# Kernel optimization log

Measured on AMD Instinct MI355X. Metric: run time of the kernel, lower is better.

Reference implementation:

```python
import jax, jax.numpy as jnp
import numpy as np

N_TOKENS = 8192
D_MODEL = 1024
D_HIDDEN = 4096
N_EXPERTS = 8
TOP_K = 2


def setup_inputs() -> dict:
    key = jax.random.key(0)
    ks = jax.random.split(key, 7)
    s = 0.02
    return {
        "x": jax.random.normal(ks[0], (N_TOKENS, D_MODEL), dtype=jnp.float32),
        "gate_w": jax.random.normal(ks[1], (D_MODEL, N_EXPERTS), dtype=jnp.float32) * s,
        "gate_b": jnp.zeros((N_EXPERTS,), dtype=jnp.float32),
        "w1": jax.random.normal(ks[2], (N_EXPERTS, D_MODEL, D_HIDDEN), dtype=jnp.float32) * s,
        "b1": jnp.zeros((N_EXPERTS, D_HIDDEN), dtype=jnp.float32),
        "w2": jax.random.normal(ks[3], (N_EXPERTS, D_HIDDEN, D_MODEL), dtype=jnp.float32) * s,
        "b2": jnp.zeros((N_EXPERTS, D_MODEL), dtype=jnp.float32),
    }


def reference(x, gate_w, gate_b, w1, b1, w2, b2):
    # Gating: softmax over experts, then top-k routing
    gate_scores = jax.nn.softmax(x @ gate_w + gate_b, axis=-1)        # [N, E]
    topk_vals, topk_idx = jax.lax.top_k(gate_scores, TOP_K)          # [N, K]

    # Combine weights: sum of topk_vals scattered to expert slots
    onehot = jax.nn.one_hot(topk_idx, N_EXPERTS, dtype=x.dtype)      # [N, K, E]
    combine = jnp.einsum('nk,nke->ne', topk_vals, onehot)            # [N, E]

    # Dense expert evaluation (math identical to masked dispatch: unselected
    # experts receive weight 0 in `combine`).
    h = jax.nn.relu(jnp.einsum('nd,edh->neh', x, w1) + b1)           # [N, E, H]
    expert_out = jnp.einsum('neh,ehd->ned', h, w2) + b2              # [N, E, D]
    output = jnp.einsum('ned,ne->nd', expert_out, combine)           # [N, D]

    # Load-balancing loss from routing counts
    load = jnp.sum(onehot, axis=(0, 1))                              # [E]
    load_balancing_loss = jnp.sum((load / jnp.sum(load)) ** 2)
    return output, load_balancing_loss
```

## Files before the change

kernel.cpp:

```cpp
#include <hip/hip_runtime.h>

#define D_MODEL   1024
#define D_HIDDEN  4096
#define N_EXPERTS 8
#define N_TOKENS  8192
#define NASSIGN   (N_TOKENS * 2)
#define PADCAP    (NASSIGN + N_EXPERTS * 256)
#define RT_TILES  (PADCAP / 256)

typedef unsigned short u16;
typedef __bf16 bf16x8 __attribute__((ext_vector_type(8)));
typedef float  f32x4  __attribute__((ext_vector_type(4)));

__device__ __forceinline__ u16 f2bf(float f) {
  union { float f; unsigned u; } c; c.f = f;
  unsigned u = c.u;
  u = (u + 0x7fffu + ((u >> 16) & 1u)) >> 16;
  return (u16)u;
}

__device__ __forceinline__ void async16(const void* g, void* l) {
  __builtin_amdgcn_global_load_lds(
      (const __attribute__((address_space(1))) unsigned int*)g,
      (__attribute__((address_space(3))) unsigned int*)l, 16, 0, 0);
}

#define MFMA(a, b, c) __builtin_amdgcn_mfma_f32_16x16x32_bf16((a), (b), (c), 0, 0, 0)

#define WAIT8_BARRIER() asm volatile("s_waitcnt vmcnt(8)\n\ts_barrier" ::: "memory")
#define WAIT0_BARRIER() asm volatile("s_waitcnt vmcnt(0)\n\ts_barrier" ::: "memory")
#define BARRIER()       asm volatile("s_barrier" ::: "memory")

__global__ __launch_bounds__(256) void gating_kernel(
    const float* __restrict__ x, const float* __restrict__ gw,
    const float* __restrict__ gb, int* __restrict__ counts,
    int* __restrict__ tok_idx, float* __restrict__ tok_w)
{
  const int n = blockIdx.x * 4 + (threadIdx.x >> 6);
  const int lane = threadIdx.x & 63;
  float acc[8] = {0.f,0.f,0.f,0.f,0.f,0.f,0.f,0.f};
  for (int d = lane; d < D_MODEL; d += 64) {
    float xv = x[(size_t)n * D_MODEL + d];
    const float4* g = (const float4*)&gw[d * 8];
    float4 g0 = g[0], g1 = g[1];
    acc[0] += xv * g0.x; acc[1] += xv * g0.y; acc[2] += xv * g0.z; acc[3] += xv * g0.w;
    acc[4] += xv * g1.x; acc[5] += xv * g1.y; acc[6] += xv * g1.z; acc[7] += xv * g1.w;
  }
  for (int off = 32; off; off >>= 1)
    #pragma unroll
    for (int e = 0; e < 8; ++e) acc[e] += __shfl_xor(acc[e], off, 64);
  if (lane == 0) {
    float l[8], p[8];
    float m = -1e30f;
    for (int e = 0; e < 8; ++e) { l[e] = acc[e] + gb[e]; m = fmaxf(m, l[e]); }
    float s = 0.f;
    for (int e = 0; e < 8; ++e) { p[e] = expf(l[e] - m); s += p[e]; }
    float inv = 1.f / s;
    for (int e = 0; e < 8; ++e) p[e] *= inv;
    int i0 = 0;
    for (int e = 1; e < 8; ++e) if (p[e] > p[i0]) i0 = e;
    int i1 = (i0 == 0) ? 1 : 0;
    for (int e = 0; e < 8; ++e) if (e != i0 && p[e] > p[i1]) i1 = e;
    tok_idx[2 * n]     = i0;  tok_idx[2 * n + 1] = i1;
    tok_w[2 * n]       = p[i0]; tok_w[2 * n + 1] = p[i1];
    atomicAdd(&counts[i0], 1);
    atomicAdd(&counts[i1], 1);
  }
}

__global__ void finalize_routing(const int* __restrict__ counts,
                                 int* __restrict__ offsets,
                                 float* __restrict__ out_loss)
{
  int off = 0;
  for (int e = 0; e < 8; ++e) {
    offsets[e] = off;
    off += ((counts[e] + 255) >> 8) << 8;
  }
  offsets[8] = off;
  float loss = 0.f;
  for (int e = 0; e < 8; ++e) {
    float f = (float)counts[e] * (1.f / (float)NASSIGN);
    loss += f * f;
  }
  *out_loss = loss;
}

__global__ __launch_bounds__(256) void scatter_kernel(
    const int* __restrict__ tok_idx, const float* __restrict__ tok_w,
    const int* __restrict__ offsets, int* __restrict__ cursors,
    int* __restrict__ assign_token, float* __restrict__ assign_w,
    int* __restrict__ tok_pos)
{
  const int n = blockIdx.x * 256 + threadIdx.x;
  #pragma unroll
  for (int k = 0; k < 2; ++k) {
    int e = tok_idx[n * 2 + k];
    int pos = offsets[e] + atomicAdd(&cursors[e], 1);
    assign_token[pos] = n;
    assign_w[pos] = tok_w[n * 2 + k];
    tok_pos[n * 2 + k] = pos;
  }
}

__global__ __launch_bounds__(256) void convert_x_kernel(
    const float* __restrict__ x, u16* __restrict__ xb)
{
  size_t i = ((size_t)blockIdx.x * 256 + threadIdx.x) * 4;
  float4 v = *(const float4*)&x[i];
  unsigned lo = (unsigned)f2bf(v.x) | ((unsigned)f2bf(v.y) << 16);
  unsigned hi = (unsigned)f2bf(v.z) | ((unsigned)f2bf(v.w) << 16);
  uint2 o; o.x = lo; o.y = hi;
  *(uint2*)&xb[i] = o;
}

__global__ __launch_bounds__(256) void transpose_cvt_kernel(
    const float* __restrict__ in, u16* __restrict__ out, int R, int C)
{
  const int e = blockIdx.z;
  const int c0 = blockIdx.x * 32, r0 = blockIdx.y * 32;
  __shared__ float tile[32][33];
  const int tx = threadIdx.x & 31, ty = threadIdx.x >> 5;
  const float* ip = in + (size_t)e * R * C;
  u16* op = out + (size_t)e * R * C;
  #pragma unroll
  for (int i = 0; i < 4; ++i)
    tile[ty + i * 8][tx] = ip[(size_t)(r0 + ty + i * 8) * C + c0 + tx];
  __syncthreads();
  #pragma unroll
  for (int i = 0; i < 4; ++i)
    op[(size_t)(c0 + ty + i * 8) * R + r0 + tx] = f2bf(tile[tx][ty + i * 8]);
}


__global__ __launch_bounds__(512, 2) void gemm1_kernel(
    const u16* __restrict__ xb, const u16* __restrict__ w1t,
    const float* __restrict__ b1, const int* __restrict__ assign_token,
    const int* __restrict__ offsets, u16* __restrict__ hbuf)
{
  const int rtl = (blockIdx.x & 7) * 9 + (blockIdx.x >> 3);
  const int ct = blockIdx.y;
  if (rtl * 256 >= offsets[8]) return;
  int e = 0;
  while (offsets[e + 1] <= rtl * 256) ++e;

  __shared__ __align__(16) u16 smem[65536];

  const int tid = threadIdx.x;
  const int wave = tid >> 6, lane = tid & 63;
  const int wm = wave >> 2, wn = wave & 3;

  const int r0 = tid >> 2, s0 = (tid & 3) ^ ((r0 >> 1) & 3);
  const int r1 = r0 + 128, s1 = (tid & 3) ^ ((r1 >> 1) & 3);
  const long aS0 = (long)assign_token[rtl * 256 + r0] * D_MODEL + s0 * 8;
  const long aS1 = (long)assign_token[rtl * 256 + r1] * D_MODEL + s1 * 8;
  const long bS0 = ((long)e * D_HIDDEN + ct * 256 + r0) * D_MODEL + s0 * 8;
  const long bS1 = ((long)e * D_HIDDEN + ct * 256 + r1) * D_MODEL + s1 * 8;

  f32x4 acc[8][4];
  #pragma unroll
  for (int i = 0; i < 8; ++i)
    #pragma unroll
    for (int j = 0; j < 4; ++j) acc[i][j] = (f32x4){0.f, 0.f, 0.f, 0.f};

  int aoff[8], boff[4];
  #pragma unroll
  for (int f = 0; f < 8; ++f) {
    int row = wm * 128 + f * 16 + (lane & 15);
    aoff[f] = row * 32 + (((lane >> 4) ^ ((row >> 1) & 3)) * 8);
  }
  #pragma unroll
  for (int f = 0; f < 4; ++f) {
    int col = wn * 64 + f * 16 + (lane & 15);
    boff[f] = 32768 + col * 32 + (((lane >> 4) ^ ((col >> 1) & 3)) * 8);
  }

  #define STG1(d, h, koff) do { \
    u16* A_ = &smem[((d) * 2 + (h)) * 8192 + wave * 512]; \
    u16* B_ = &smem[32768 + ((d) * 2 + (h)) * 8192 + wave * 512]; \
    async16(xb  + aS0 + (koff), A_); \
    async16(xb  + aS1 + (koff), A_ + 4096); \
    async16(w1t + bS0 + (koff), B_); \
    async16(w1t + bS1 + (koff), B_ + 4096); \
  } while (0)

  const int NT = D_MODEL / 64;
  STG1(0, 0, 0);
  STG1(0, 1, 32);
  STG1(1, 0, 64);

  for (int t = 0; t < NT; ++t) {
    const int d = t & 1;
    const int reg0 = d * 16384, reg1 = d * 16384 + 8192;
    bf16x8 a[8], b0, b1r;
    if (t + 1 < NT) WAIT8_BARRIER();
    else            WAIT0_BARRIER();
    #pragma unroll
    for (int f = 0; f < 8; ++f) a[f] = *(const bf16x8*)&smem[reg0 + aoff[f]];
    b0 = *(const bf16x8*)&smem[reg0 + boff[0]];
    b1r = *(const bf16x8*)&smem[reg0 + boff[1]];
    if (t + 1 < NT) STG1(d ^ 1, 1, (t + 1) * 64 + 32);
    __builtin_amdgcn_s_setprio(1);
    #pragma unroll
    for (int f = 0; f < 8; ++f) {
      acc[f][0] = MFMA(a[f], b0, acc[f][0]);
      acc[f][1] = MFMA(a[f], b1r, acc[f][1]);
    }
    __builtin_amdgcn_s_setprio(0);
    BARRIER();
    b0 = *(const bf16x8*)&smem[reg0 + boff[2]];
    b1r = *(const bf16x8*)&smem[reg0 + boff[3]];
    __builtin_amdgcn_s_setprio(1);
    #pragma unroll
    for (int f = 0; f < 8; ++f) {
      acc[f][2] = MFMA(a[f], b0, acc[f][2]);
      acc[f][3] = MFMA(a[f], b1r, acc[f][3]);
    }
    __builtin_amdgcn_s_setprio(0);
    if (t + 1 < NT) WAIT8_BARRIER();
    else            WAIT0_BARRIER();
    #pragma unroll
    for (int f = 0; f < 8; ++f) a[f] = *(const bf16x8*)&smem[reg1 + aoff[f]];
    b0 = *(const bf16x8*)&smem[reg1 + boff[0]];
    b1r = *(const bf16x8*)&smem[reg1 + boff[1]];
    if (t + 2 < NT) STG1(d, 0, (t + 2) * 64);
    __builtin_amdgcn_s_setprio(1);
    #pragma unroll
    for (int f = 0; f < 8; ++f) {
      acc[f][0] = MFMA(a[f], b0, acc[f][0]);
      acc[f][1] = MFMA(a[f], b1r, acc[f][1]);
    }
    __builtin_amdgcn_s_setprio(0);
    BARRIER();
    b0 = *(const bf16x8*)&smem[reg1 + boff[2]];
    b1r = *(const bf16x8*)&smem[reg1 + boff[3]];
    __builtin_amdgcn_s_setprio(1);
    #pragma unroll
    for (int f = 0; f < 8; ++f) {
      acc[f][2] = MFMA(a[f], b0, acc[f][2]);
      acc[f][3] = MFMA(a[f], b1r, acc[f][3]);
    }
    __builtin_amdgcn_s_setprio(0);
  }
  #undef STG1

  float bias[4];
  #pragma unroll
  for (int j = 0; j < 4; ++j)
    bias[j] = b1[(size_t)e * D_HIDDEN + ct * 256 + wn * 64 + j * 16 + (lane & 15)];

  __syncthreads();
  u16* Hs = smem;
  #pragma unroll
  for (int i = 0; i < 8; ++i)
    #pragma unroll
    for (int j = 0; j < 4; ++j)
      #pragma unroll
      for (int r = 0; r < 4; ++r) {
        int rl = wm * 128 + i * 16 + ((lane >> 4) * 4) + r;
        int cl = wn * 64 + j * 16 + (lane & 15);
        Hs[rl * 256 + cl] = f2bf(fmaxf(acc[i][j][r] + bias[j], 0.f));
      }
  __syncthreads();
  #pragma unroll
  for (int it = 0; it < 16; ++it) {
    int cc = tid + it * 512;
    int row = cc >> 5, cs = cc & 31;
    *(uint4*)&hbuf[((size_t)(rtl * 256 + row)) * D_HIDDEN + ct * 256 + cs * 8] =
        *(const uint4*)&Hs[row * 256 + cs * 8];
  }
}

template <bool EO>
__global__ __launch_bounds__(512, 2) void gemm2_kernel(
    const u16* __restrict__ hbuf, const u16* __restrict__ w2t,
    const float* __restrict__ b2, const int* __restrict__ assign_token,
    const float* __restrict__ assign_w, const int* __restrict__ offsets,
    float* __restrict__ dst)
{
  const int rtl = (blockIdx.x & 7) * 9 + (blockIdx.x >> 3);
  const int ct = blockIdx.y;
  const int sk = blockIdx.z;
  const long skb = (long)sk * 1024;
  if (rtl * 256 >= offsets[8]) return;
  int e = 0;
  while (offsets[e + 1] <= rtl * 256) ++e;

  __shared__ __align__(16) u16 smem[65536];

  const int tid = threadIdx.x;
  const int wave = tid >> 6, lane = tid & 63;
  const int wm = wave >> 2, wn = wave & 3;

  const int r0 = tid >> 2, s0 = (tid & 3) ^ ((r0 >> 1) & 3);
  const int r1 = r0 + 128, s1 = (tid & 3) ^ ((r1 >> 1) & 3);
  const long aS0 = ((long)(rtl * 256 + r0)) * D_HIDDEN + s0 * 8;
  const long aS1 = ((long)(rtl * 256 + r1)) * D_HIDDEN + s1 * 8;
  const long bS0 = ((long)e * D_MODEL + ct * 256 + r0) * D_HIDDEN + s0 * 8;
  const long bS1 = ((long)e * D_MODEL + ct * 256 + r1) * D_HIDDEN + s1 * 8;

  f32x4 acc[8][4];
  #pragma unroll
  for (int i = 0; i < 8; ++i)
    #pragma unroll
    for (int j = 0; j < 4; ++j) acc[i][j] = (f32x4){0.f, 0.f, 0.f, 0.f};

  int aoff[8], boff[4];
  #pragma unroll
  for (int f = 0; f < 8; ++f) {
    int row = wm * 128 + f * 16 + (lane & 15);
    aoff[f] = row * 32 + (((lane >> 4) ^ ((row >> 1) & 3)) * 8);
  }
  #pragma unroll
  for (int f = 0; f < 4; ++f) {
    int col = wn * 64 + f * 16 + (lane & 15);
    boff[f] = 32768 + col * 32 + (((lane >> 4) ^ ((col >> 1) & 3)) * 8);
  }

  #define STG2(d, h, koff) do { \
    u16* A_ = &smem[((d) * 2 + (h)) * 8192 + wave * 512]; \
    u16* B_ = &smem[32768 + ((d) * 2 + (h)) * 8192 + wave * 512]; \
    async16(hbuf + aS0 + (koff), A_); \
    async16(hbuf + aS1 + (koff), A_ + 4096); \
    async16(w2t + bS0 + (koff), B_); \
    async16(w2t + bS1 + (koff), B_ + 4096); \
  } while (0)

  const int NT = 1024 / 64;
  STG2(0, 0, skb);
  STG2(0, 1, skb + 32);
  STG2(1, 0, skb + 64);

  for (int t = 0; t < NT; ++t) {
    const int d = t & 1;
    const int reg0 = d * 16384, reg1 = d * 16384 + 8192;
    bf16x8 a[8], b0, b1r;
    if (t + 1 < NT) WAIT8_BARRIER();
    else            WAIT0_BARRIER();
    #pragma unroll
    for (int f = 0; f < 8; ++f) a[f] = *(const bf16x8*)&smem[reg0 + aoff[f]];
    b0 = *(const bf16x8*)&smem[reg0 + boff[0]];
    b1r = *(const bf16x8*)&smem[reg0 + boff[1]];
    if (t + 1 < NT) STG2(d ^ 1, 1, skb + (t + 1) * 64 + 32);
    __builtin_amdgcn_s_setprio(1);
    #pragma unroll
    for (int f = 0; f < 8; ++f) {
      acc[f][0] = MFMA(a[f], b0, acc[f][0]);
      acc[f][1] = MFMA(a[f], b1r, acc[f][1]);
    }
    __builtin_amdgcn_s_setprio(0);
    BARRIER();
    b0 = *(const bf16x8*)&smem[reg0 + boff[2]];
    b1r = *(const bf16x8*)&smem[reg0 + boff[3]];
    __builtin_amdgcn_s_setprio(1);
    #pragma unroll
    for (int f = 0; f < 8; ++f) {
      acc[f][2] = MFMA(a[f], b0, acc[f][2]);
      acc[f][3] = MFMA(a[f], b1r, acc[f][3]);
    }
    __builtin_amdgcn_s_setprio(0);
    if (t + 1 < NT) WAIT8_BARRIER();
    else            WAIT0_BARRIER();
    #pragma unroll
    for (int f = 0; f < 8; ++f) a[f] = *(const bf16x8*)&smem[reg1 + aoff[f]];
    b0 = *(const bf16x8*)&smem[reg1 + boff[0]];
    b1r = *(const bf16x8*)&smem[reg1 + boff[1]];
    if (t + 2 < NT) STG2(d, 0, skb + (t + 2) * 64);
    __builtin_amdgcn_s_setprio(1);
    #pragma unroll
    for (int f = 0; f < 8; ++f) {
      acc[f][0] = MFMA(a[f], b0, acc[f][0]);
      acc[f][1] = MFMA(a[f], b1r, acc[f][1]);
    }
    __builtin_amdgcn_s_setprio(0);
    BARRIER();
    b0 = *(const bf16x8*)&smem[reg1 + boff[2]];
    b1r = *(const bf16x8*)&smem[reg1 + boff[3]];
    __builtin_amdgcn_s_setprio(1);
    #pragma unroll
    for (int f = 0; f < 8; ++f) {
      acc[f][2] = MFMA(a[f], b0, acc[f][2]);
      acc[f][3] = MFMA(a[f], b1r, acc[f][3]);
    }
    __builtin_amdgcn_s_setprio(0);
  }
  #undef STG2

  float bias[4];
  #pragma unroll
  for (int j = 0; j < 4; ++j)
    bias[j] = (sk == 0) ? b2[(size_t)e * D_MODEL + ct * 256 + wn * 64 + j * 16 + (lane & 15)] : 0.f;

  __syncthreads();
  float* wsm = (float*)smem;
  int* tsm = (int*)&smem[1024];
  if (tid < 256) {
    wsm[tid] = assign_w[rtl * 256 + tid];
    tsm[tid] = assign_token[rtl * 256 + tid];
  }
  __syncthreads();

  #pragma unroll
  for (int i = 0; i < 8; ++i)
    #pragma unroll
    for (int r = 0; r < 4; ++r) {
      int rl = wm * 128 + i * 16 + ((lane >> 4) * 4) + r;
      float wgt = wsm[rl];
      if (EO) {
        size_t row = (size_t)(rtl * 256 + rl);
        #pragma unroll
        for (int j = 0; j < 4; ++j) {
          float v = (acc[i][j][r] + bias[j]) * wgt;
          atomicAdd(&dst[row * D_MODEL + ct * 256 + wn * 64 + j * 16 + (lane & 15)], v);
        }
      } else {
        int tok = tsm[rl];
        #pragma unroll
        for (int j = 0; j < 4; ++j) {
          float v = (acc[i][j][r] + bias[j]) * wgt;
          atomicAdd(&dst[(size_t)tok * D_MODEL + ct * 256 + wn * 64 + j * 16 + (lane & 15)], v);
        }
      }
    }
}

__global__ __launch_bounds__(256) void combine_kernel(
    const float* __restrict__ eo, const int* __restrict__ tok_pos,
    float* __restrict__ out)
{
  int idx = blockIdx.x * 256 + threadIdx.x;
  int n = idx >> 8;
  int c = (idx & 255) * 4;
  int p0 = tok_pos[2 * n], p1 = tok_pos[2 * n + 1];
  float4 a = *(const float4*)&eo[(size_t)p0 * D_MODEL + c];
  float4 b = *(const float4*)&eo[(size_t)p1 * D_MODEL + c];
  float4 o; o.x = a.x + b.x; o.y = a.y + b.y; o.z = a.z + b.z; o.w = a.w + b.w;
  *(float4*)&out[(size_t)n * D_MODEL + c] = o;
}

__global__ __launch_bounds__(256) void moe_fallback_kernel(
    const float* __restrict__ x, const float* __restrict__ w1,
    const float* __restrict__ b1, const float* __restrict__ w2,
    const float* __restrict__ b2, const int* __restrict__ tok_idx,
    const float* __restrict__ tok_w, float* __restrict__ out)
{
  const int a = blockIdx.x;
  const int n = a >> 1, slot = a & 1;
  const int e = tok_idx[n * 2 + slot];
  const float wgt = tok_w[n * 2 + slot];
  __shared__ float xs[D_MODEL];
  __shared__ float hs[D_HIDDEN];
  const int tid = threadIdx.x;
  for (int d = tid; d < D_MODEL; d += 256) xs[d] = x[(size_t)n * D_MODEL + d];
  __syncthreads();
  for (int h = tid; h < D_HIDDEN; h += 256) {
    float acc = b1[(size_t)e * D_HIDDEN + h];
    for (int d = 0; d < D_MODEL; ++d)
      acc += xs[d] * w1[((size_t)e * D_MODEL + d) * D_HIDDEN + h];
    hs[h] = fmaxf(acc, 0.f);
  }
  __syncthreads();
  for (int d = tid; d < D_MODEL; d += 256) {
    float acc = b2[(size_t)e * D_MODEL + d];
    for (int h = 0; h < D_HIDDEN; ++h)
      acc += hs[h] * w2[((size_t)e * D_HIDDEN + h) * D_MODEL + d];
    atomicAdd(&out[(size_t)n * D_MODEL + d], wgt * acc);
  }
}

extern "C" void kernel_launch(void* const* d_in, const int* in_sizes, int n_in,
                              void* d_out, int out_size, void* d_ws, size_t ws_size,
                              hipStream_t stream) {
  const float* x      = (const float*)d_in[0];
  const float* gate_w = (const float*)d_in[1];
  const float* gate_b = (const float*)d_in[2];
  const float* w1     = (const float*)d_in[3];
  const float* b1     = (const float*)d_in[4];
  const float* w2     = (const float*)d_in[5];
  const float* b2     = (const float*)d_in[6];
  float* out = (float*)d_out;

  char* ws = (char*)d_ws;
  int*   counts       = (int*)(ws + 0);
  int*   cursors      = (int*)(ws + 32);
  int*   offsets      = (int*)(ws + 64);
  int*   tok_idx      = (int*)(ws + 256);
  float* tok_w        = (float*)(ws + 65792);
  int*   tok_pos      = (int*)(ws + 131328);
  int*   assign_token = (int*)(ws + 196864);
  float* assign_w     = (float*)(ws + 270592);
  const size_t X0 = 344320;
  u16*   hbuf = (u16*)(ws + X0);
  u16*   xb   = (u16*)(ws + X0 + 150994944ull);
  u16*   w1t  = (u16*)(ws + X0 + 150994944ull + 16777216ull);
  u16*   w2t  = (u16*)(ws + X0 + 150994944ull);
  float* eo   = (float*)(ws + X0 + 150994944ull + 67108864ull);
  const size_t REQ_FAST = X0 + 150994944ull + 16777216ull + 67108864ull;
  const size_t REQ_EO   = X0 + 150994944ull + 67108864ull + 75497472ull;

  const bool fast = (ws_size >= REQ_FAST);
  const bool eoPath = fast && (ws_size >= REQ_EO);

  hipMemsetAsync(ws, 0, X0, stream);
  if (!eoPath) {
    hipMemsetAsync(d_out, 0, (size_t)out_size * sizeof(float), stream);
  }

  gating_kernel<<<N_TOKENS / 4, 256, 0, stream>>>(x, gate_w, gate_b, counts, tok_idx, tok_w);
  finalize_routing<<<1, 1, 0, stream>>>(counts, offsets, out + (out_size - 1));

  if (fast) {
    scatter_kernel<<<N_TOKENS / 256, 256, 0, stream>>>(tok_idx, tok_w, offsets, cursors,
                                                       assign_token, assign_w, tok_pos);
    convert_x_kernel<<<(N_TOKENS * D_MODEL) / 1024, 256, 0, stream>>>(x, xb);
    transpose_cvt_kernel<<<dim3(D_HIDDEN / 32, D_MODEL / 32, N_EXPERTS), 256, 0, stream>>>(
        w1, w1t, D_MODEL, D_HIDDEN);
    gemm1_kernel<<<dim3(RT_TILES, D_HIDDEN / 256), 512, 0, stream>>>(
        xb, w1t, b1, assign_token, offsets, hbuf);
    transpose_cvt_kernel<<<dim3(D_MODEL / 32, D_HIDDEN / 32, N_EXPERTS), 256, 0, stream>>>(
        w2, w2t, D_HIDDEN, D_MODEL);
    if (eoPath) {
      hipMemsetAsync(eo, 0, 75497472ull, stream);
      gemm2_kernel<true><<<dim3(RT_TILES, D_MODEL / 256, 4), 512, 0, stream>>>(
          hbuf, w2t, b2, assign_token, assign_w, offsets, eo);
      combine_kernel<<<(N_TOKENS * D_MODEL) / 1024, 256, 0, stream>>>(eo, tok_pos, out);
    } else {
      gemm2_kernel<false><<<dim3(RT_TILES, D_MODEL / 256, 4), 512, 0, stream>>>(
          hbuf, w2t, b2, assign_token, assign_w, offsets, out);
    }
  } else {
    moe_fallback_kernel<<<NASSIGN, 256, 0, stream>>>(x, w1, b1, w2, b2, tok_idx, tok_w, out);
  }
}
```

Baseline: 886.7 us.

## Rework GEMM pipeline barriers and halve gemm2 split-K factor

Restructures the main loop of both GEMM kernels: the wait threshold drops from vmcnt(8) to vmcnt(4), each half-stage uses separate B fragment registers (b2/b3), and extra barriers separate LDS reads from the MFMA phases and the next async stage. Gemm2's split-K factor goes from 4 to 2, so each block covers 2048 of the K dimension. The aim is tighter load/compute interleaving and fewer partial-sum atomics or stores in gemm2. The cost is more barriers per iteration and fewer gemm2 blocks, which could reduce occupancy or latency hiding.

```diff
diff --git a/kernel.cpp b/kernel.cpp
--- a/kernel.cpp
+++ b/kernel.cpp
@@ -27,7 +27,7 @@
 
 #define MFMA(a, b, c) __builtin_amdgcn_mfma_f32_16x16x32_bf16((a), (b), (c), 0, 0, 0)
 
-#define WAIT8_BARRIER() asm volatile("s_waitcnt vmcnt(8)\n\ts_barrier" ::: "memory")
+#define WAIT4_BARRIER() asm volatile("s_waitcnt vmcnt(4)\n\ts_barrier" ::: "memory")
 #define WAIT0_BARRIER() asm volatile("s_waitcnt vmcnt(0)\n\ts_barrier" ::: "memory")
 #define BARRIER()       asm volatile("s_barrier" ::: "memory")
 
@@ -188,18 +188,18 @@
   STG1(0, 0, 0);
   STG1(0, 1, 32);
   STG1(1, 0, 64);
+  WAIT4_BARRIER();
 
   for (int t = 0; t < NT; ++t) {
     const int d = t & 1;
     const int reg0 = d * 16384, reg1 = d * 16384 + 8192;
-    bf16x8 a[8], b0, b1r;
-    if (t + 1 < NT) WAIT8_BARRIER();
-    else            WAIT0_BARRIER();
+    bf16x8 a[8], b0, b1r, b2, b3;
     #pragma unroll
     for (int f = 0; f < 8; ++f) a[f] = *(const bf16x8*)&smem[reg0 + aoff[f]];
-    b0 = *(const bf16x8*)&smem[reg0 + boff[0]];
+    b0  = *(const bf16x8*)&smem[reg0 + boff[0]];
     b1r = *(const bf16x8*)&smem[reg0 + boff[1]];
     if (t + 1 < NT) STG1(d ^ 1, 1, (t + 1) * 64 + 32);
+    BARRIER();
     __builtin_amdgcn_s_setprio(1);
     #pragma unroll
     for (int f = 0; f < 8; ++f) {
@@ -208,22 +208,23 @@
     }
     __builtin_amdgcn_s_setprio(0);
     BARRIER();
-    b0 = *(const bf16x8*)&smem[reg0 + boff[2]];
-    b1r = *(const bf16x8*)&smem[reg0 + boff[3]];
-    __builtin_amdgcn_s_setprio(1);
-    #pragma unroll
-    for (int f = 0; f < 8; ++f) {
-      acc[f][2] = MFMA(a[f], b0, acc[f][2]);
-      acc[f][3] = MFMA(a[f], b1r, acc[f][3]);
-    }
-    __builtin_amdgcn_s_setprio(0);
-    if (t + 1 < NT) WAIT8_BARRIER();
-    else            WAIT0_BARRIER();
+    b2 = *(const bf16x8*)&smem[reg0 + boff[2]];
+    b3 = *(const bf16x8*)&smem[reg0 + boff[3]];
+    BARRIER();
+    __builtin_amdgcn_s_setprio(1);
+    #pragma unroll
+    for (int f = 0; f < 8; ++f) {
+      acc[f][2] = MFMA(a[f], b2, acc[f][2]);
+      acc[f][3] = MFMA(a[f], b3, acc[f][3]);
+    }
+    __builtin_amdgcn_s_setprio(0);
+    BARRIER();
     #pragma unroll
     for (int f = 0; f < 8; ++f) a[f] = *(const bf16x8*)&smem[reg1 + aoff[f]];
-    b0 = *(const bf16x8*)&smem[reg1 + boff[0]];
+    b0  = *(const bf16x8*)&smem[reg1 + boff[0]];
     b1r = *(const bf16x8*)&smem[reg1 + boff[1]];
     if (t + 2 < NT) STG1(d, 0, (t + 2) * 64);
+    BARRIER();
     __builtin_amdgcn_s_setprio(1);
     #pragma unroll
     for (int f = 0; f < 8; ++f) {
@@ -232,15 +233,18 @@
     }
     __builtin_amdgcn_s_setprio(0);
     BARRIER();
-    b0 = *(const bf16x8*)&smem[reg1 + boff[2]];
-    b1r = *(const bf16x8*)&smem[reg1 + boff[3]];
-    __builtin_amdgcn_s_setprio(1);
-    #pragma unroll
-    for (int f = 0; f < 8; ++f) {
-      acc[f][2] = MFMA(a[f], b0, acc[f][2]);
-      acc[f][3] = MFMA(a[f], b1r, acc[f][3]);
-    }
-    __builtin_amdgcn_s_setprio(0);
+    b2 = *(const bf16x8*)&smem[reg1 + boff[2]];
+    b3 = *(const bf16x8*)&smem[reg1 + boff[3]];
+    if (t < NT - 2) WAIT4_BARRIER();
+    else            WAIT0_BARRIER();
+    __builtin_amdgcn_s_setprio(1);
+    #pragma unroll
+    for (int f = 0; f < 8; ++f) {
+      acc[f][2] = MFMA(a[f], b2, acc[f][2]);
+      acc[f][3] = MFMA(a[f], b3, acc[f][3]);
+    }
+    __builtin_amdgcn_s_setprio(0);
+    BARRIER();
   }
   #undef STG1
 
@@ -281,7 +285,7 @@
   const int rtl = (blockIdx.x & 7) * 9 + (blockIdx.x >> 3);
   const int ct = blockIdx.y;
   const int sk = blockIdx.z;
-  const long skb = (long)sk * 1024;
+  const long skb = (long)sk * 2048;
   if (rtl * 256 >= offsets[8]) return;
   int e = 0;
   while (offsets[e + 1] <= rtl * 256) ++e;
@@ -326,22 +330,22 @@
     async16(w2t + bS1 + (koff), B_ + 4096); \
   } while (0)
 
-  const int NT = 1024 / 64;
+  const int NT = 2048 / 64;
   STG2(0, 0, skb);
   STG2(0, 1, skb + 32);
   STG2(1, 0, skb + 64);
+  WAIT4_BARRIER();
 
   for (int t = 0; t < NT; ++t) {
     const int d = t & 1;
     const int reg0 = d * 16384, reg1 = d * 16384 + 8192;
-    bf16x8 a[8], b0, b1r;
-    if (t + 1 < NT) WAIT8_BARRIER();
-    else            WAIT0_BARRIER();
+    bf16x8 a[8], b0, b1r, b2, b3;
     #pragma unroll
     for (int f = 0; f < 8; ++f) a[f] = *(const bf16x8*)&smem[reg0 + aoff[f]];
-    b0 = *(const bf16x8*)&smem[reg0 + boff[0]];
+    b0  = *(const bf16x8*)&smem[reg0 + boff[0]];
     b1r = *(const bf16x8*)&smem[reg0 + boff[1]];
     if (t + 1 < NT) STG2(d ^ 1, 1, skb + (t + 1) * 64 + 32);
+    BARRIER();
     __builtin_amdgcn_s_setprio(1);
     #pragma unroll
     for (int f = 0; f < 8; ++f) {
@@ -350,22 +354,23 @@
     }
     __builtin_amdgcn_s_setprio(0);
     BARRIER();
-    b0 = *(const bf16x8*)&smem[reg0 + boff[2]];
-    b1r = *(const bf16x8*)&smem[reg0 + boff[3]];
-    __builtin_amdgcn_s_setprio(1);
-    #pragma unroll
-    for (int f = 0; f < 8; ++f) {
-      acc[f][2] = MFMA(a[f], b0, acc[f][2]);
-      acc[f][3] = MFMA(a[f], b1r, acc[f][3]);
-    }
-    __builtin_amdgcn_s_setprio(0);
-    if (t + 1 < NT) WAIT8_BARRIER();
-    else            WAIT0_BARRIER();
+    b2 = *(const bf16x8*)&smem[reg0 + boff[2]];
+    b3 = *(const bf16x8*)&smem[reg0 + boff[3]];
+    BARRIER();
+    __builtin_amdgcn_s_setprio(1);
+    #pragma unroll
+    for (int f = 0; f < 8; ++f) {
+      acc[f][2] = MFMA(a[f], b2, acc[f][2]);
+      acc[f][3] = MFMA(a[f], b3, acc[f][3]);
+    }
+    __builtin_amdgcn_s_setprio(0);
+    BARRIER();
     #pragma unroll
     for (int f = 0; f < 8; ++f) a[f] = *(const bf16x8*)&smem[reg1 + aoff[f]];
-    b0 = *(const bf16x8*)&smem[reg1 + boff[0]];
+    b0  = *(const bf16x8*)&smem[reg1 + boff[0]];
     b1r = *(const bf16x8*)&smem[reg1 + boff[1]];
     if (t + 2 < NT) STG2(d, 0, skb + (t + 2) * 64);
+    BARRIER();
     __builtin_amdgcn_s_setprio(1);
     #pragma unroll
     for (int f = 0; f < 8; ++f) {
@@ -374,15 +379,18 @@
     }
     __builtin_amdgcn_s_setprio(0);
     BARRIER();
-    b0 = *(const bf16x8*)&smem[reg1 + boff[2]];
-    b1r = *(const bf16x8*)&smem[reg1 + boff[3]];
-    __builtin_amdgcn_s_setprio(1);
-    #pragma unroll
-    for (int f = 0; f < 8; ++f) {
-      acc[f][2] = MFMA(a[f], b0, acc[f][2]);
-      acc[f][3] = MFMA(a[f], b1r, acc[f][3]);
-    }
-    __builtin_amdgcn_s_setprio(0);
+    b2 = *(const bf16x8*)&smem[reg1 + boff[2]];
+    b3 = *(const bf16x8*)&smem[reg1 + boff[3]];
+    if (t < NT - 2) WAIT4_BARRIER();
+    else            WAIT0_BARRIER();
+    __builtin_amdgcn_s_setprio(1);
+    #pragma unroll
+    for (int f = 0; f < 8; ++f) {
+      acc[f][2] = MFMA(a[f], b2, acc[f][2]);
+      acc[f][3] = MFMA(a[f], b3, acc[f][3]);
+    }
+    __builtin_amdgcn_s_setprio(0);
+    BARRIER();
   }
   #undef STG2
 
@@ -521,11 +529,11 @@
         w2, w2t, D_HIDDEN, D_MODEL);
     if (eoPath) {
       hipMemsetAsync(eo, 0, 75497472ull, stream);
-      gemm2_kernel<true><<<dim3(RT_TILES, D_MODEL / 256, 4), 512, 0, stream>>>(
+      gemm2_kernel<true><<<dim3(RT_TILES, D_MODEL / 256, 2), 512, 0, stream>>>(
           hbuf, w2t, b2, assign_token, assign_w, offsets, eo);
       combine_kernel<<<(N_TOKENS * D_MODEL) / 1024, 256, 0, stream>>>(eo, tok_pos, out);
     } else {
-      gemm2_kernel<false><<<dim3(RT_TILES, D_MODEL / 256, 4), 512, 0, stream>>>(
+      gemm2_kernel<false><<<dim3(RT_TILES, D_MODEL / 256, 2), 512, 0, stream>>>(
           hbuf, w2t, b2, assign_token, assign_w, offsets, out);
     }
   } else {
```

After: 846.6 us. 1.05x faster.
